# Kernel tuning notes

Measured on AMD Instinct MI355X. Metric: run time of the kernel, lower is better.

Reference implementation:

```python
import jax, jax.numpy as jnp
import numpy as np

# Model dims (from init_kwargs + mamba_ssm defaults)
D_MODEL = 1024
N_LAYER = 2
D_STATE = 16
D_CONV = 4
D_INNER = 2 * D_MODEL          # expand=2
DT_RANK = D_MODEL // 16        # 64
VOCAB = 32000
BATCH, SEQLEN = 2, 1024


def setup_inputs() -> dict:
    key = jax.random.key(0)
    ks = jax.random.split(key, 10)
    s = 0.02
    x = jax.random.randint(ks[0], (BATCH, SEQLEN), 0, VOCAB)
    embedding = jax.random.normal(ks[1], (VOCAB, D_MODEL), dtype=jnp.float32) * s
    norm_w = jnp.ones((N_LAYER, D_MODEL), dtype=jnp.float32)
    in_proj_w = jax.random.normal(ks[2], (N_LAYER, 2 * D_INNER, D_MODEL), dtype=jnp.float32) * s
    conv_w = jax.random.normal(ks[3], (N_LAYER, D_INNER, D_CONV), dtype=jnp.float32) * (1.0 / np.sqrt(D_CONV))
    conv_b = jnp.zeros((N_LAYER, D_INNER), dtype=jnp.float32)
    x_proj_w = jax.random.normal(ks[4], (N_LAYER, DT_RANK + 2 * D_STATE, D_INNER), dtype=jnp.float32) * s
    dt_proj_w = jax.random.normal(ks[5], (N_LAYER, D_INNER, DT_RANK), dtype=jnp.float32) * (DT_RANK ** -0.5)
    # inverse-softplus of dt_init ~ 0.01 (mamba default dt range)
    dt_bias = jnp.full((N_LAYER, D_INNER), float(np.log(np.expm1(0.01))), dtype=jnp.float32)
    A_log = jnp.log(jnp.broadcast_to(jnp.arange(1, D_STATE + 1, dtype=jnp.float32), (N_LAYER, D_INNER, D_STATE)))
    D = jnp.ones((N_LAYER, D_INNER), dtype=jnp.float32)
    out_proj_w = jax.random.normal(ks[6], (N_LAYER, D_MODEL, D_INNER), dtype=jnp.float32) * s
    final_norm_w = jnp.ones((D_MODEL,), dtype=jnp.float32)
    return {"x": x, "embedding": embedding, "norm_w": norm_w, "in_proj_w": in_proj_w,
            "conv_w": conv_w, "conv_b": conv_b, "x_proj_w": x_proj_w, "dt_proj_w": dt_proj_w,
            "dt_bias": dt_bias, "A_log": A_log, "D": D, "out_proj_w": out_proj_w,
            "final_norm_w": final_norm_w}


def _rmsnorm(h, w, eps=1e-5):
    return h * jax.lax.rsqrt(jnp.mean(h * h, axis=-1, keepdims=True) + eps) * w


def _scan_combine(c1, c2):
    a1, b1 = c1
    a2, b2 = c2
    return a2 * a1, a2 * b1 + b2


def _mamba_block(h, norm_w, in_proj_w, conv_w, conv_b, x_proj_w, dt_proj_w, dt_bias, A_log, D, out_proj_w):
    u = _rmsnorm(h, norm_w)
    xz = jnp.einsum('bld,ed->ble', u, in_proj_w)           # [B,L,2*D_INNER]
    xi, z = jnp.split(xz, 2, axis=-1)
    # depthwise causal conv1d, kernel D_CONV
    k = conv_w.T[:, None, :]                               # [D_CONV, 1, D_INNER]
    xc = jax.lax.conv_general_dilated(xi, k, (1,), [(D_CONV - 1, 0)],
                                      dimension_numbers=('NLC', 'LIO', 'NLC'),
                                      feature_group_count=D_INNER) + conv_b
    xc = jax.nn.silu(xc)
    dbl = jnp.einsum('bld,ed->ble', xc, x_proj_w)          # [B,L,DT_RANK+2*D_STATE]
    dt_low = dbl[..., :DT_RANK]
    Bm = dbl[..., DT_RANK:DT_RANK + D_STATE]
    Cm = dbl[..., DT_RANK + D_STATE:]
    dt = jax.nn.softplus(jnp.einsum('blr,dr->bld', dt_low, dt_proj_w) + dt_bias)
    A = -jnp.exp(A_log)                                    # [D_INNER, D_STATE]
    a = jnp.exp(dt[..., None] * A)                         # [B,L,D_INNER,D_STATE]
    b = dt[..., None] * Bm[:, :, None, :] * xc[..., None]  # [B,L,D_INNER,D_STATE]
    hs = jax.lax.associative_scan(_scan_combine, (a, b), axis=1)[1]
    y = jnp.einsum('bldn,bln->bld', hs, Cm) + xc * D
    y = y * jax.nn.silu(z)
    return h + jnp.einsum('bld,md->blm', y, out_proj_w)


def reference(x, embedding, norm_w, in_proj_w, conv_w, conv_b, x_proj_w, dt_proj_w,
              dt_bias, A_log, D, out_proj_w, final_norm_w):
    h = embedding[x]                                       # [B,L,D_MODEL]
    for i in range(N_LAYER):
        h = _mamba_block(h, norm_w[i], in_proj_w[i], conv_w[i], conv_b[i], x_proj_w[i],
                         dt_proj_w[i], dt_bias[i], A_log[i], D[i], out_proj_w[i])
    h = _rmsnorm(h, final_norm_w)
    logits = jnp.einsum('bld,vd->blv', h, embedding)       # tied lm head
    return logits
```

## Files before the change

### kernel.cpp

```cpp
#include <hip/hip_runtime.h>
#include <hip/hip_bf16.h>
#include <math.h>

#define D_MODEL 1024
#define N_LAYER 2
#define D_STATE 16
#define D_CONV  4
#define D_INNER 2048
#define DT_RANK 64
#define VOCAB   32000
#define BATCH   2
#define SEQLEN  1024
#define TOKENS  (BATCH*SEQLEN)
#define NC      32
#define CL      32

typedef __hip_bfloat16 bf16;
typedef __bf16 bf16x8 __attribute__((ext_vector_type(8)));
typedef float f32x4 __attribute__((ext_vector_type(4)));

__device__ inline void gld_lds16(const bf16* g, bf16* l) {
    __builtin_amdgcn_global_load_lds(
        (const __attribute__((address_space(1))) void*)g,
        (__attribute__((address_space(3))) void*)l, 16, 0, 0);
}

__device__ inline float softplus_fast(float v) {
    return (v > 20.f) ? v : __logf(1.f + __expf(v));
}
__device__ inline float silu_fast(float v) {
    return v / (1.f + __expf(-v));
}

__global__ __launch_bounds__(256) void embed_kernel(const int* __restrict__ x,
                                                    const float* __restrict__ emb,
                                                    float* __restrict__ h) {
    int t = blockIdx.x;
    int tok = x[t];
    const float4* src = (const float4*)(emb + (size_t)tok * D_MODEL);
    float4* dst = (float4*)(h + (size_t)t * D_MODEL);
    dst[threadIdx.x] = src[threadIdx.x];
}

__global__ __launch_bounds__(256) void rmsnorm_bf16(const float* __restrict__ h,
                                                    const float* __restrict__ w,
                                                    bf16* __restrict__ u) {
    int t = blockIdx.x;
    const float4* hv = (const float4*)(h + (size_t)t * D_MODEL);
    float4 v = hv[threadIdx.x];
    float ss = v.x*v.x + v.y*v.y + v.z*v.z + v.w*v.w;
    #pragma unroll
    for (int off = 32; off > 0; off >>= 1) ss += __shfl_down(ss, off);
    __shared__ float red[4];
    int lane = threadIdx.x & 63, wid = threadIdx.x >> 6;
    if (lane == 0) red[wid] = ss;
    __syncthreads();
    float tot = red[0] + red[1] + red[2] + red[3];
    float scale = rsqrtf(tot * (1.0f / (float)D_MODEL) + 1e-5f);
    float4 wq = ((const float4*)w)[threadIdx.x];
    size_t o = (size_t)t * D_MODEL + threadIdx.x * 4;
    u[o+0] = __float2bfloat16(v.x * scale * wq.x);
    u[o+1] = __float2bfloat16(v.y * scale * wq.y);
    u[o+2] = __float2bfloat16(v.z * scale * wq.z);
    u[o+3] = __float2bfloat16(v.w * scale * wq.w);
}

__global__ __launch_bounds__(256) void f32_to_bf16(const float* __restrict__ s,
                                                   bf16* __restrict__ d, int n) {
    int i = (blockIdx.x * 256 + threadIdx.x) * 4;
    if (i < n) {
        float4 v = *(const float4*)(s + i);
        d[i+0] = __float2bfloat16(v.x);
        d[i+1] = __float2bfloat16(v.y);
        d[i+2] = __float2bfloat16(v.z);
        d[i+3] = __float2bfloat16(v.w);
    }
}

__global__ __launch_bounds__(256) void conv_xproj_pad(const float* __restrict__ s,
                                                      bf16* __restrict__ d) {
    int col = blockIdx.x * 256 + threadIdx.x;
    int row = blockIdx.y;
    int layer = blockIdx.z;
    float v = (row < 96) ? s[((size_t)layer * 96 + row) * D_INNER + col] : 0.f;
    d[((size_t)layer * 128 + row) * D_INNER + col] = __float2bfloat16(v);
}

__global__ __launch_bounds__(256) void gemm_bf16(
    const bf16* __restrict__ A, int lda,
    const bf16* __restrict__ W, int ldw,
    float* __restrict__ C, int ldc,
    int N, int K, int acc, int swz, int M, int bfout)
{
    __shared__ bf16 lds[2][2][128 * 64];
    int bx = blockIdx.x, by = blockIdx.y;
    if (swz) {
        int bid = by * gridDim.x + bx;
        int q = (gridDim.x * gridDim.y) >> 3;
        int n = (bid & 7) * q + (bid >> 3);
        by = n % gridDim.y;
        bx = n / gridDim.y;
    }
    const int z = blockIdx.z;
    A += (size_t)z * K;
    W += (size_t)z * K;
    C += (size_t)z * M * (size_t)ldc;

    const int tid  = threadIdx.x;
    const int wave = tid >> 6;
    const int lane = tid & 63;
    const int wr = wave >> 1, wc = wave & 1;
    const size_t rowBase = (size_t)by * 128;
    const size_t colBase = (size_t)bx * 128;

    const int srow = 8 * wave + (lane >> 3);
    const int scol = ((lane & 7) ^ (lane >> 3)) << 3;
    const bf16* aGs = A + (rowBase + srow) * (size_t)lda + scol;
    const bf16* bGs = W + (colBase + srow) * (size_t)ldw + scol;

#define STAGE(tt, bb) do {                                                      \
        const size_t kofs_ = (size_t)(tt) * 64;                                 \
        _Pragma("unroll")                                                       \
        for (int i_ = 0; i_ < 4; ++i_) {                                        \
            gld_lds16(aGs + kofs_ + (size_t)(32 * i_) * lda,                    \
                      &lds[bb][0][(32 * i_ + 8 * wave) * 64]);                  \
            gld_lds16(bGs + kofs_ + (size_t)(32 * i_) * ldw,                    \
                      &lds[bb][1][(32 * i_ + 8 * wave) * 64]);                  \
        }                                                                       \
    } while (0)

    f32x4 accv[4][4];
    #pragma unroll
    for (int i = 0; i < 4; ++i)
        #pragma unroll
        for (int j = 0; j < 4; ++j)
            accv[i][j] = f32x4{0.f, 0.f, 0.f, 0.f};

    const int arow0 = wr * 64 + (lane & 15);
    const int brow0 = wc * 64 + (lane & 15);
    const int h8  = (lane >> 4) << 3;
    const int sw8 = (lane & 7) << 3;

    const int NT = K >> 6;
    STAGE(0, 0);
    for (int t = 0; t < NT; ++t) {
        const int cur = t & 1;
        if (t + 1 < NT) {
            STAGE(t + 1, cur ^ 1);
            asm volatile("s_waitcnt vmcnt(8)" ::: "memory");
        } else {
            asm volatile("s_waitcnt vmcnt(0)" ::: "memory");
        }
        __builtin_amdgcn_s_barrier();

        const bf16* Ab = &lds[cur][0][0];
        const bf16* Bb = &lds[cur][1][0];
        #pragma unroll
        for (int kk = 0; kk < 2; ++kk) {
            const int cs = ((kk << 5) + h8) ^ sw8;
            bf16x8 af[4], bv[4];
            #pragma unroll
            for (int i = 0; i < 4; ++i)
                af[i] = *(const bf16x8*)(Ab + (arow0 + 16 * i) * 64 + cs);
            #pragma unroll
            for (int j = 0; j < 4; ++j)
                bv[j] = *(const bf16x8*)(Bb + (brow0 + 16 * j) * 64 + cs);
            #pragma unroll
            for (int i = 0; i < 4; ++i)
                #pragma unroll
                for (int j = 0; j < 4; ++j)
                    accv[i][j] = __builtin_amdgcn_mfma_f32_16x16x32_bf16(
                        af[i], bv[j], accv[i][j], 0, 0, 0);
        }
        asm volatile("s_waitcnt lgkmcnt(0)" ::: "memory");
        __builtin_amdgcn_s_barrier();
    }
#undef STAGE

    const int cl = lane & 15;
    const int rg = (lane >> 4) * 4;
    #pragma unroll
    for (int i = 0; i < 4; ++i) {
        #pragma unroll
        for (int j = 0; j < 4; ++j) {
            int col = (int)colBase + wc * 64 + j * 16 + cl;
            if (col < N) {
                size_t base = (rowBase + wr * 64 + i * 16 + rg) * (size_t)ldc + col;
                if (bfout) {
                    bf16* Cb = (bf16*)C;
                    #pragma unroll
                    for (int r = 0; r < 4; ++r)
                        Cb[base + (size_t)r * ldc] = __float2bfloat16(accv[i][j][r]);
                } else {
                    #pragma unroll
                    for (int r = 0; r < 4; ++r) {
                        size_t idx = base + (size_t)r * ldc;
                        C[idx] = acc ? C[idx] + accv[i][j][r] : accv[i][j][r];
                    }
                }
            }
        }
    }
}

__global__ __launch_bounds__(512) void gemm_vocab_w(
    const bf16* __restrict__ A,
    const bf16* __restrict__ W,
    float* __restrict__ C)
{
    __shared__ bf16 ldsA[2][256 * 32];
    __shared__ bf16 ldsB[2][128 * 32];
    int bx = blockIdx.x, by = blockIdx.y;
    {
        int bid = by * gridDim.x + bx;
        int n = (bid & 7) * ((gridDim.x * gridDim.y) >> 3) + (bid >> 3);
        by = n & 7;
        bx = n >> 3;
    }
    const int tid  = threadIdx.x;
    const int wave = tid >> 6;
    const int lane = tid & 63;
    const int wr = wave >> 1;
    const int wc = wave & 1;
    const size_t rowBase = (size_t)by * 256;
    const size_t colBase = (size_t)bx * 128;

    const int srow   = lane >> 2;
    const int schunk = ((lane & 3) ^ ((lane >> 3) & 3)) << 3;
    const bf16* aG0 = A + (rowBase + 16 * wave       + srow) * (size_t)D_MODEL + schunk;
    const bf16* aG1 = A + (rowBase + 128 + 16 * wave + srow) * (size_t)D_MODEL + schunk;
    const bf16* bG  = W + (colBase + 16 * wave       + srow) * (size_t)D_MODEL + schunk;

#define STAGEW(tt, bb) do {                                                     \
        const size_t ko_ = (size_t)(tt) * 32;                                   \
        gld_lds16(aG0 + ko_, &ldsA[bb][512 * wave]);                            \
        gld_lds16(aG1 + ko_, &ldsA[bb][512 * (8 + wave)]);                      \
        gld_lds16(bG  + ko_, &ldsB[bb][512 * wave]);                            \
    } while (0)

    f32x4 accv[4][4];
    #pragma unroll
    for (int i = 0; i < 4; ++i)
        #pragma unroll
        for (int j = 0; j < 4; ++j)
            accv[i][j] = f32x4{0.f, 0.f, 0.f, 0.f};

    const int l15 = lane & 15;
    const int cs = (((lane >> 4) ^ ((l15 >> 1) & 3)) << 3);
    const int arow0 = wr * 64 + l15;
    const int brow0 = wc * 64 + l15;

    STAGEW(0, 0);
    #pragma unroll 1
    for (int t = 0; t < 32; ++t) {
        const int cur = t & 1;
        if (t + 1 < 32) {
            STAGEW(t + 1, cur ^ 1);
            asm volatile("s_waitcnt vmcnt(3)" ::: "memory");
        } else {
            asm volatile("s_waitcnt vmcnt(0)" ::: "memory");
        }
        __builtin_amdgcn_s_barrier();

        const bf16* Ab = &ldsA[cur][0];
        const bf16* Bb = &ldsB[cur][0];
        bf16x8 af[4], bv[4];
        #pragma unroll
        for (int i = 0; i < 4; ++i)
            af[i] = *(const bf16x8*)(Ab + (arow0 + 16 * i) * 32 + cs);
        #pragma unroll
        for (int j = 0; j < 4; ++j)
            bv[j] = *(const bf16x8*)(Bb + (brow0 + 16 * j) * 32 + cs);
        #pragma unroll
        for (int i = 0; i < 4; ++i)
            #pragma unroll
            for (int j = 0; j < 4; ++j)
                accv[i][j] = __builtin_amdgcn_mfma_f32_16x16x32_bf16(
                    af[i], bv[j], accv[i][j], 0, 0, 0);

        asm volatile("s_waitcnt lgkmcnt(0)" ::: "memory");
        __builtin_amdgcn_s_barrier();
    }
#undef STAGEW

    const int cl = l15;
    const int rg = (lane >> 4) * 4;
    #pragma unroll
    for (int i = 0; i < 4; ++i) {
        #pragma unroll
        for (int j = 0; j < 4; ++j) {
            int col = (int)colBase + wc * 64 + j * 16 + cl;
            size_t base = (rowBase + wr * 64 + i * 16 + rg) * (size_t)VOCAB + col;
            #pragma unroll
            for (int r = 0; r < 4; ++r)
                C[base + (size_t)r * VOCAB] = accv[i][j][r];
        }
    }
}

__global__ __launch_bounds__(256) void conv_silu_kernel(const bf16* __restrict__ xz,
                                                        const float* __restrict__ cw,
                                                        const float* __restrict__ cb,
                                                        float* __restrict__ xcf,
                                                        bf16* __restrict__ xcb) {
    int d = blockIdx.x * 256 + threadIdx.x;
    int l0 = blockIdx.y * 8;
    int b = blockIdx.z;
    float w0 = cw[d*4+0], w1 = cw[d*4+1], w2 = cw[d*4+2], w3 = cw[d*4+3];
    float bias = cb[d];
    float win0 = (l0 >= 3) ? __bfloat162float(xz[((size_t)b * SEQLEN + l0 - 3) * (2*D_INNER) + d]) : 0.f;
    float win1 = (l0 >= 2) ? __bfloat162float(xz[((size_t)b * SEQLEN + l0 - 2) * (2*D_INNER) + d]) : 0.f;
    float win2 = (l0 >= 1) ? __bfloat162float(xz[((size_t)b * SEQLEN + l0 - 1) * (2*D_INNER) + d]) : 0.f;
    #pragma unroll
    for (int i = 0; i < 8; ++i) {
        float cur = __bfloat162float(xz[((size_t)b * SEQLEN + l0 + i) * (2*D_INNER) + d]);
        float acc = bias + w0*win0 + w1*win1 + w2*win2 + w3*cur;
        float s = silu_fast(acc);
        size_t o = ((size_t)b * SEQLEN + l0 + i) * D_INNER + d;
        xcf[o] = s;
        xcb[o] = __float2bfloat16(s);
        win0 = win1; win1 = win2; win2 = cur;
    }
}

__global__ __launch_bounds__(256) void reduce_xproj(const float* __restrict__ px,
                                                    float* __restrict__ dblf,
                                                    bf16* __restrict__ dbl_b) {
    int i = blockIdx.x * 256 + threadIdx.x;
    float s = 0.f;
    #pragma unroll
    for (int z = 0; z < 8; ++z) s += px[(size_t)z * (TOKENS*96) + i];
    dblf[i] = s;
    dbl_b[i] = __float2bfloat16(s);
}

__global__ __launch_bounds__(256) void reduce_oproj(const float* __restrict__ po,
                                                    float* __restrict__ h) {
    int i = (blockIdx.x * 256 + threadIdx.x) * 4;
    float4 a = *(const float4*)(po + i);
    float4 b = *(const float4*)(po + (size_t)TOKENS*D_MODEL + i);
    float4 hv = *(const float4*)(h + i);
    hv.x += a.x + b.x; hv.y += a.y + b.y; hv.z += a.z + b.z; hv.w += a.w + b.w;
    *(float4*)(h + i) = hv;
}

__global__ __launch_bounds__(256) void scan_chunk(const float* __restrict__ dtp,
                                                  const float* __restrict__ dt_bias,
                                                  const float* __restrict__ dbl,
                                                  const float* __restrict__ xc,
                                                  const float* __restrict__ A_log,
                                                  float* __restrict__ aprod,
                                                  float* __restrict__ sfin) {
    int d = blockIdx.x * 256 + threadIdx.x;
    int c = blockIdx.y;
    int b = blockIdx.z;
    __shared__ float Bs[CL][D_STATE];
    for (int i = threadIdx.x; i < CL * D_STATE; i += 256) {
        int l = i >> 4, n = i & 15;
        Bs[l][n] = dbl[((size_t)b * SEQLEN + c * CL + l) * 96 + DT_RANK + n];
    }
    __syncthreads();
    float A[D_STATE];
    #pragma unroll
    for (int n = 0; n < D_STATE; ++n) A[n] = -__expf(A_log[d * D_STATE + n]);
    float bias = dt_bias[d];
    float st[D_STATE];
    #pragma unroll
    for (int n = 0; n < D_STATE; ++n) st[n] = 0.f;
    float dts = 0.f;
    for (int l = 0; l < CL; ++l) {
        size_t t = (size_t)b * SEQLEN + c * CL + l;
        float dtv = softplus_fast(dtp[t * D_INNER + d] + bias);
        dts += dtv;
        float dx = dtv * xc[t * D_INNER + d];
        #pragma unroll
        for (int n = 0; n < D_STATE; ++n) {
            float a = __expf(dtv * A[n]);
            st[n] = a * st[n] + dx * Bs[l][n];
        }
    }
    #pragma unroll
    for (int n = 0; n < D_STATE; ++n) {
        size_t o = (((size_t)b * NC + c) * D_STATE + n) * D_INNER + d;
        aprod[o] = __expf(dts * A[n]);
        sfin[o] = st[n];
    }
}

__global__ __launch_bounds__(256) void scan_carry(const float* __restrict__ aprod,
                                                  const float* __restrict__ sfin,
                                                  float* __restrict__ initS) {
    int idx = blockIdx.x * 256 + threadIdx.x;
    int d = idx & (D_INNER - 1);
    int n = (idx >> 11) & (D_STATE - 1);
    int b = idx >> 15;
    float st = 0.f;
    for (int c = 0; c < NC; ++c) {
        size_t o = (((size_t)b * NC + c) * D_STATE + n) * D_INNER + d;
        initS[o] = st;
        st = aprod[o] * st + sfin[o];
    }
}

__global__ __launch_bounds__(256) void scan_emit(const float* __restrict__ dtp,
                                                 const float* __restrict__ dt_bias,
                                                 const float* __restrict__ dbl,
                                                 const float* __restrict__ xc,
                                                 const bf16* __restrict__ xz,
                                                 const float* __restrict__ A_log,
                                                 const float* __restrict__ Dp,
                                                 const float* __restrict__ initS,
                                                 bf16* __restrict__ y) {
    int d = blockIdx.x * 256 + threadIdx.x;
    int c = blockIdx.y;
    int b = blockIdx.z;
    __shared__ float BCs[CL][2 * D_STATE];
    for (int i = threadIdx.x; i < CL * 2 * D_STATE; i += 256) {
        int l = i >> 5, n = i & 31;
        BCs[l][n] = dbl[((size_t)b * SEQLEN + c * CL + l) * 96 + DT_RANK + n];
    }
    __syncthreads();
    float A[D_STATE];
    #pragma unroll
    for (int n = 0; n < D_STATE; ++n) A[n] = -__expf(A_log[d * D_STATE + n]);
    float bias = dt_bias[d];
    float Dv = Dp[d];
    float st[D_STATE];
    #pragma unroll
    for (int n = 0; n < D_STATE; ++n)
        st[n] = initS[(((size_t)b * NC + c) * D_STATE + n) * D_INNER + d];
    for (int l = 0; l < CL; ++l) {
        size_t t = (size_t)b * SEQLEN + c * CL + l;
        float dtv = softplus_fast(dtp[t * D_INNER + d] + bias);
        float xcv = xc[t * D_INNER + d];
        float dx = dtv * xcv;
        float acc = 0.f;
        #pragma unroll
        for (int n = 0; n < D_STATE; ++n) {
            float a = __expf(dtv * A[n]);
            st[n] = a * st[n] + dx * BCs[l][n];
            acc += st[n] * BCs[l][D_STATE + n];
        }
        acc += xcv * Dv;
        float zv = __bfloat162float(xz[t * (2 * D_INNER) + D_INNER + d]);
        y[t * D_INNER + d] = __float2bfloat16(acc * silu_fast(zv));
    }
}

extern "C" void kernel_launch(void* const* d_in, const int* in_sizes, int n_in,
                              void* d_out, int out_size, void* d_ws, size_t ws_size,
                              hipStream_t stream) {
    const int*   x          = (const int*)  d_in[0];
    const float* emb        = (const float*)d_in[1];
    const float* norm_w     = (const float*)d_in[2];
    const float* in_proj_w  = (const float*)d_in[3];
    const float* conv_w     = (const float*)d_in[4];
    const float* conv_b     = (const float*)d_in[5];
    const float* x_proj_w   = (const float*)d_in[6];
    const float* dt_proj_w  = (const float*)d_in[7];
    const float* dt_bias    = (const float*)d_in[8];
    const float* A_log      = (const float*)d_in[9];
    const float* Dp         = (const float*)d_in[10];
    const float* out_proj_w = (const float*)d_in[11];
    const float* fnorm_w    = (const float*)d_in[12];
    float* out = (float*)d_out;
    float* ws  = (float*)d_ws;

    bf16*  embf   = (bf16*)ws;
    bf16*  u_b    = (bf16*)(ws + 16384000);
    bf16*  xz_b   = (bf16*)(ws + 17432576);
    float* xc_f   = ws + 25821184;
    bf16*  xc_b   = (bf16*)(ws + 30015488);
    float* dtp    = ws + 32112640;
    float* h      = ws + 36306944;
    float* dblf   = ws + 38404096;
    bf16*  dbl_b  = (bf16*)(ws + 38600704);
    bf16*  y_b    = (bf16*)(ws + 38699008);
    bf16*  inpj_b = (bf16*)(ws + 40796160);
    bf16*  xpj_b  = (bf16*)(ws + 44990464);
    bf16*  dtpj_b = (bf16*)(ws + 45252608);
    bf16*  otpj_b = (bf16*)(ws + 45383680);
    float* aprod  = ws + 47480832;
    float* sfin   = ws + 49577984;
    float* initS  = ws + 51675136;
    float* px     = ws + 53772288;
    float* po     = ws + 55345152;

    f32_to_bf16<<<(VOCAB*D_MODEL/4 + 255)/256, 256, 0, stream>>>(emb, embf, VOCAB*D_MODEL);
    f32_to_bf16<<<(2*2*D_INNER*D_MODEL/4 + 255)/256, 256, 0, stream>>>(in_proj_w,  inpj_b, 2*2*D_INNER*D_MODEL);
    conv_xproj_pad<<<dim3(D_INNER/256, 128, N_LAYER), 256, 0, stream>>>(x_proj_w, xpj_b);
    f32_to_bf16<<<(2*D_INNER*DT_RANK/4 + 255)/256, 256, 0, stream>>>(dt_proj_w,  dtpj_b, 2*D_INNER*DT_RANK);
    f32_to_bf16<<<(2*D_MODEL*D_INNER/4 + 255)/256, 256, 0, stream>>>(out_proj_w, otpj_b, 2*D_MODEL*D_INNER);

    embed_kernel<<<TOKENS, 256, 0, stream>>>(x, emb, h);

    for (int layer = 0; layer < N_LAYER; ++layer) {
        rmsnorm_bf16<<<TOKENS, 256, 0, stream>>>(h, norm_w + layer * D_MODEL, u_b);
        gemm_bf16<<<dim3(4096/128, TOKENS/128), 256, 0, stream>>>(
            u_b, D_MODEL, inpj_b + (size_t)layer * 2 * D_INNER * D_MODEL, D_MODEL,
            (float*)xz_b, 2 * D_INNER, 2 * D_INNER, D_MODEL, 0, 1, TOKENS, 1);
        conv_silu_kernel<<<dim3(D_INNER/256, SEQLEN/8, BATCH), 256, 0, stream>>>(
            xz_b, conv_w + (size_t)layer * D_INNER * D_CONV, conv_b + layer * D_INNER,
            xc_f, xc_b);
        gemm_bf16<<<dim3(1, TOKENS/128, 8), 256, 0, stream>>>(
            xc_b, D_INNER, xpj_b + (size_t)layer * 128 * D_INNER, D_INNER,
            px, 96, 96, 256, 0, 0, TOKENS, 0);
        reduce_xproj<<<(TOKENS*96)/256, 256, 0, stream>>>(px, dblf, dbl_b);
        gemm_bf16<<<dim3(D_INNER/128, TOKENS/128), 256, 0, stream>>>(
            dbl_b, 96, dtpj_b + (size_t)layer * D_INNER * DT_RANK, DT_RANK,
            dtp, D_INNER, D_INNER, DT_RANK, 0, 1, TOKENS, 0);
        scan_chunk<<<dim3(D_INNER/256, NC, BATCH), 256, 0, stream>>>(
            dtp, dt_bias + layer * D_INNER, dblf, xc_f,
            A_log + (size_t)layer * D_INNER * D_STATE, aprod, sfin);
        scan_carry<<<(BATCH*D_STATE*D_INNER)/256, 256, 0, stream>>>(aprod, sfin, initS);
        scan_emit<<<dim3(D_INNER/256, NC, BATCH), 256, 0, stream>>>(
            dtp, dt_bias + layer * D_INNER, dblf, xc_f, xz_b,
            A_log + (size_t)layer * D_INNER * D_STATE, Dp + layer * D_INNER,
            initS, y_b);
        gemm_bf16<<<dim3(D_MODEL/128, TOKENS/128, 2), 256, 0, stream>>>(
            y_b, D_INNER, otpj_b + (size_t)layer * D_MODEL * D_INNER, D_INNER,
            po, D_MODEL, D_MODEL, 1024, 0, 1, TOKENS, 0);
        reduce_oproj<<<(TOKENS*D_MODEL/4)/256, 256, 0, stream>>>(po, h);
    }

    rmsnorm_bf16<<<TOKENS, 256, 0, stream>>>(h, fnorm_w, u_b);

    gemm_vocab_w<<<dim3(VOCAB/128, TOKENS/256), 512, 0, stream>>>(u_b, embf, out);
}
```

Baseline: 531.1 us.

## Triple-buffer vocab GEMM with BK=64 and interleaved prefetch across MFMA phases

Rewrites the LM-head GEMM main loop to use a K-tile of 64 with three LDS buffers, prefetching two tiles ahead and splitting each tile's global-to-LDS loads into two halves interleaved with the two MFMA sub-steps. The trailing per-iteration barrier is dropped, and s_setprio plus sched_barrier hints are added around the MFMA blocks. The aim is to hide global-load latency and halve the barrier count. The cost is LDS use rising from 48KB to 144KB per block and a new XOR swizzle whose correctness depends on the buffer-reuse distance.

```diff
diff --git a/kernel.cpp b/kernel.cpp
--- a/kernel.cpp
+++ b/kernel.cpp
@@ -203,13 +203,13 @@
     }
 }
 
-__global__ __launch_bounds__(512) void gemm_vocab_w(
+__global__ __launch_bounds__(512) void gemm_vocab_8p(
     const bf16* __restrict__ A,
     const bf16* __restrict__ W,
     float* __restrict__ C)
 {
-    __shared__ bf16 ldsA[2][256 * 32];
-    __shared__ bf16 ldsB[2][128 * 32];
+    __shared__ bf16 sA[3][256 * 64];
+    __shared__ bf16 sB[3][128 * 64];
     int bx = blockIdx.x, by = blockIdx.y;
     {
         int bid = by * gridDim.x + bx;
@@ -225,17 +225,22 @@
     const size_t rowBase = (size_t)by * 256;
     const size_t colBase = (size_t)bx * 128;
 
-    const int srow   = lane >> 2;
-    const int schunk = ((lane & 3) ^ ((lane >> 3) & 3)) << 3;
-    const bf16* aG0 = A + (rowBase + 16 * wave       + srow) * (size_t)D_MODEL + schunk;
-    const bf16* aG1 = A + (rowBase + 128 + 16 * wave + srow) * (size_t)D_MODEL + schunk;
-    const bf16* bG  = W + (colBase + 16 * wave       + srow) * (size_t)D_MODEL + schunk;
-
-#define STAGEW(tt, bb) do {                                                     \
-        const size_t ko_ = (size_t)(tt) * 32;                                   \
-        gld_lds16(aG0 + ko_, &ldsA[bb][512 * wave]);                            \
-        gld_lds16(aG1 + ko_, &ldsA[bb][512 * (8 + wave)]);                      \
-        gld_lds16(bG  + ko_, &ldsB[bb][512 * wave]);                            \
+    const int sa = lane >> 3;
+    const int sc = ((lane & 7) ^ sa) << 3;
+    const bf16* aGs = A + (rowBase + 8 * wave + sa) * (size_t)D_MODEL + sc;
+    const bf16* bGs = W + (colBase + 8 * wave + sa) * (size_t)D_MODEL + sc;
+
+#define STAGE_P0(kt_, sAp, sBp) do {                                            \
+        const size_t ko_ = (size_t)(kt_) * 64;                                  \
+        gld_lds16(aGs + ko_,                            (sAp) + (8*wave)*64);   \
+        gld_lds16(aGs + ko_ + (size_t)64  * D_MODEL,    (sAp) + (64  + 8*wave)*64); \
+        gld_lds16(bGs + ko_,                            (sBp) + (8*wave)*64);   \
+    } while (0)
+#define STAGE_P1(kt_, sAp, sBp) do {                                            \
+        const size_t ko_ = (size_t)(kt_) * 64;                                  \
+        gld_lds16(aGs + ko_ + (size_t)128 * D_MODEL,    (sAp) + (128 + 8*wave)*64); \
+        gld_lds16(aGs + ko_ + (size_t)192 * D_MODEL,    (sAp) + (192 + 8*wave)*64); \
+        gld_lds16(bGs + ko_ + (size_t)64  * D_MODEL,    (sBp) + (64  + 8*wave)*64); \
     } while (0)
 
     f32x4 accv[4][4];
@@ -245,43 +250,76 @@
         for (int j = 0; j < 4; ++j)
             accv[i][j] = f32x4{0.f, 0.f, 0.f, 0.f};
 
-    const int l15 = lane & 15;
-    const int cs = (((lane >> 4) ^ ((l15 >> 1) & 3)) << 3);
+    const int l15  = lane & 15;
+    const int h8   = (lane >> 4) << 3;
+    const int sw8  = (lane & 7) << 3;
     const int arow0 = wr * 64 + l15;
     const int brow0 = wc * 64 + l15;
 
-    STAGEW(0, 0);
+    STAGE_P0(0, &sA[0][0], &sB[0][0]);
+    STAGE_P1(0, &sA[0][0], &sB[0][0]);
+    STAGE_P0(1, &sA[1][0], &sB[1][0]);
+    STAGE_P1(1, &sA[1][0], &sB[1][0]);
+
+    int rs = 0, ps = 2;
     #pragma unroll 1
-    for (int t = 0; t < 32; ++t) {
-        const int cur = t & 1;
-        if (t + 1 < 32) {
-            STAGEW(t + 1, cur ^ 1);
-            asm volatile("s_waitcnt vmcnt(3)" ::: "memory");
-        } else {
-            asm volatile("s_waitcnt vmcnt(0)" ::: "memory");
-        }
+    for (int kt = 0; kt < 16; ++kt) {
+        if (kt < 15) { asm volatile("s_waitcnt vmcnt(6)" ::: "memory"); }
+        else         { asm volatile("s_waitcnt vmcnt(0)" ::: "memory"); }
         __builtin_amdgcn_s_barrier();
-
-        const bf16* Ab = &ldsA[cur][0];
-        const bf16* Bb = &ldsB[cur][0];
-        bf16x8 af[4], bv[4];
-        #pragma unroll
-        for (int i = 0; i < 4; ++i)
-            af[i] = *(const bf16x8*)(Ab + (arow0 + 16 * i) * 32 + cs);
-        #pragma unroll
-        for (int j = 0; j < 4; ++j)
-            bv[j] = *(const bf16x8*)(Bb + (brow0 + 16 * j) * 32 + cs);
-        #pragma unroll
-        for (int i = 0; i < 4; ++i)
+        __builtin_amdgcn_sched_barrier(0);
+
+        const bf16* sAr = &sA[rs][0];
+        const bf16* sBr = &sB[rs][0];
+        bf16* sAp = &sA[ps][0];
+        bf16* sBp = &sB[ps][0];
+        const bool pf = (kt + 2 < 16);
+
+        if (pf) STAGE_P0(kt + 2, sAp, sBp);
+        {
+            const int cs = h8 ^ sw8;
+            bf16x8 af[4], bv[4];
+            #pragma unroll
+            for (int i = 0; i < 4; ++i)
+                af[i] = *(const bf16x8*)(sAr + (arow0 + 16 * i) * 64 + cs);
             #pragma unroll
             for (int j = 0; j < 4; ++j)
-                accv[i][j] = __builtin_amdgcn_mfma_f32_16x16x32_bf16(
-                    af[i], bv[j], accv[i][j], 0, 0, 0);
-
+                bv[j] = *(const bf16x8*)(sBr + (brow0 + 16 * j) * 64 + cs);
+            __builtin_amdgcn_s_setprio(1);
+            #pragma unroll
+            for (int i = 0; i < 4; ++i)
+                #pragma unroll
+                for (int j = 0; j < 4; ++j)
+                    accv[i][j] = __builtin_amdgcn_mfma_f32_16x16x32_bf16(
+                        af[i], bv[j], accv[i][j], 0, 0, 0);
+            __builtin_amdgcn_s_setprio(0);
+        }
+        if (pf) STAGE_P1(kt + 2, sAp, sBp);
+        {
+            const int cs = (32 + h8) ^ sw8;
+            bf16x8 af[4], bv[4];
+            #pragma unroll
+            for (int i = 0; i < 4; ++i)
+                af[i] = *(const bf16x8*)(sAr + (arow0 + 16 * i) * 64 + cs);
+            #pragma unroll
+            for (int j = 0; j < 4; ++j)
+                bv[j] = *(const bf16x8*)(sBr + (brow0 + 16 * j) * 64 + cs);
+            __builtin_amdgcn_s_setprio(1);
+            #pragma unroll
+            for (int i = 0; i < 4; ++i)
+                #pragma unroll
+                for (int j = 0; j < 4; ++j)
+                    accv[i][j] = __builtin_amdgcn_mfma_f32_16x16x32_bf16(
+                        af[i], bv[j], accv[i][j], 0, 0, 0);
+            __builtin_amdgcn_s_setprio(0);
+        }
         asm volatile("s_waitcnt lgkmcnt(0)" ::: "memory");
-        __builtin_amdgcn_s_barrier();
-    }
-#undef STAGEW
+        __builtin_amdgcn_sched_barrier(0);
+        rs = (rs == 2) ? 0 : rs + 1;
+        ps = (ps == 2) ? 0 : ps + 1;
+    }
+#undef STAGE_P0
+#undef STAGE_P1
 
     const int cl = l15;
     const int rg = (lane >> 4) * 4;
@@ -525,5 +563,5 @@
 
     rmsnorm_bf16<<<TOKENS, 256, 0, stream>>>(h, fnorm_w, u_b);
 
-    gemm_vocab_w<<<dim3(VOCAB/128, TOKENS/256), 512, 0, stream>>>(u_b, embf, out);
-}
+    gemm_vocab_8p<<<dim3(VOCAB/128, TOKENS/256), 512, 0, stream>>>(u_b, embf, out);
+}
```

New measurement: 617.9 us. 16.4% more time.
